# Kernel optimization log

Hardware: AMD Instinct MI355X
Metric: run time of the kernel (lower is better)

Reference implementation:

```python
import jax, jax.numpy as jnp
import numpy as np

B, T, E, H = 2, 2048, 4096, 32
D = E // H
NEG = -1e4  # additive causal mask value


def setup_inputs() -> dict:
    key = jax.random.key(0)
    ks = jax.random.split(key, 10)
    i8 = lambda k, shape: jax.random.randint(k, shape, -128, 128, dtype=jnp.int8)
    hidden_states = i8(ks[0], (B, T, E))
    W_q, b_q = i8(ks[1], (E, E)), i8(ks[2], (E,))
    W_k, b_k = i8(ks[3], (E, E)), i8(ks[4], (E,))
    W_v, b_v = i8(ks[5], (E, E)), i8(ks[6], (E,))
    W_o = i8(ks[7], (E, E))
    b_o = jax.random.normal(ks[8], (E,), jnp.float32)
    causal = jnp.where(jnp.tril(jnp.ones((T, T), bool)), 0.0, NEG).astype(jnp.float32)
    attention_mask = jnp.broadcast_to(causal[None, None], (B, 1, T, T))
    return {
        'hidden_states': hidden_states,
        'W_q': W_q, 'b_q': b_q, 'W_k': W_k, 'b_k': b_k,
        'W_v': W_v, 'b_v': b_v, 'W_o': W_o, 'b_o': b_o,
        'attention_mask': attention_mask,
        # dequant scales chosen so int8 outputs stay in range
        'a_q': jnp.float32(1e-4), 'a_k': jnp.float32(1e-4), 'a_v': jnp.float32(1e-4),
        'a_qk': jnp.float32(2e-5), 'a_pv': jnp.float32(1e-2), 'a_o': jnp.float32(1e-3),
    }


def _w8a8b8o8(x_i8, W_i8, b_i8, alpha):
    # int8 GEMM, int32 accumulate, fused scale+int8 bias, saturate to int8
    acc = jnp.einsum('bte,oe->bto', x_i8.astype(jnp.int32), W_i8.astype(jnp.int32))
    y = acc.astype(jnp.float32) * alpha + b_i8.astype(jnp.float32)
    return jnp.clip(jnp.round(y), -128, 127).astype(jnp.int8)


def _heads(x):  # [B,T,E] -> [B,H,T,D]
    return x.reshape(B, T, H, D).transpose(0, 2, 1, 3)


def reference(hidden_states, W_q, b_q, W_k, b_k, W_v, b_v, W_o, b_o,
              attention_mask, a_q, a_k, a_v, a_qk, a_pv, a_o):
    q = _heads(_w8a8b8o8(hidden_states, W_q, b_q, a_q))
    k = _heads(_w8a8b8o8(hidden_states, W_k, b_k, a_k))
    v = _heads(_w8a8b8o8(hidden_states, W_v, b_v, a_v))

    # BMM_S8T_S8N_F32T: fp32 logits = a_qk * int32(q @ k^T)
    logits = a_qk * jnp.einsum('bhtd,bhsd->bhts',
                               q.astype(jnp.int32), k.astype(jnp.int32)).astype(jnp.float32)
    logits = logits + attention_mask  # broadcast over heads
    probs = jax.nn.softmax(logits, axis=-1)
    p_i8 = jnp.round(probs * 127.0).astype(jnp.int8)  # attn_probs.mul_(127).round_()

    # BMM_S8T_S8N_S8T: int8 ctx = sat(round(a_pv * int32(p @ v)))
    ctx_acc = jnp.einsum('bhts,bhsd->bhtd',
                         p_i8.astype(jnp.int32), v.astype(jnp.int32)).astype(jnp.float32)
    ctx = jnp.clip(jnp.round(a_pv * ctx_acc), -128, 127).astype(jnp.int8)
    ctx = ctx.transpose(0, 2, 1, 3).reshape(B, T, E)

    # W8A8BFP32OFP32: fp32 out = a_o * int32(ctx @ W_o^T) + b_o
    out_acc = jnp.einsum('bte,oe->bto',
                         ctx.astype(jnp.int32), W_o.astype(jnp.int32)).astype(jnp.float32)
    return a_o * out_acc + b_o
```

## Files before the change

kernel.cpp:

```cpp
#include <hip/hip_runtime.h>

#define Bdim 2
#define Tdim 2048
#define Edim 4096
#define Hdim 32
#define Ddim 128
#define Mdim (Bdim*Tdim)
#define Kdim 4096

typedef int v4i __attribute__((ext_vector_type(4)));

__device__ __forceinline__ void glds16(const void* g, void* l) {
  __builtin_amdgcn_global_load_lds(
      (const __attribute__((address_space(1))) void*)g,
      (__attribute__((address_space(3))) void*)l, 16, 0, 0);
}

__global__ __launch_bounds__(256) void pack5_kernel(
    const int* __restrict__ s0, const int* __restrict__ s1, const int* __restrict__ s2,
    const int* __restrict__ s3, const int* __restrict__ s4,
    char* __restrict__ d0, char* __restrict__ d1, char* __restrict__ d2,
    char* __restrict__ d3, char* __restrict__ d4) {
  int which = blockIdx.y;
  const int* s = which == 0 ? s0 : which == 1 ? s1 : which == 2 ? s2 : which == 3 ? s3 : s4;
  char* d = which == 0 ? d0 : which == 1 ? d1 : which == 2 ? d2 : which == 3 ? d3 : d4;
  int i = blockIdx.x * 256 + threadIdx.x;
  int4 x = ((const int4*)s)[i];
  char4 y; y.x = (char)x.x; y.y = (char)x.y; y.z = (char)x.z; y.w = (char)x.w;
  ((char4*)d)[i] = y;
}

__global__ __launch_bounds__(256) void transpose_v(const char* __restrict__ V8,
                                                   char* __restrict__ Vt) {
  int bh = blockIdx.z, b = bh >> 5, h = bh & 31;
  int s0 = blockIdx.x * 64, d0 = blockIdx.y * 64;
  __shared__ __align__(16) char tl[64 * 80];
  int idx = threadIdx.x;
  {
    int row = idx >> 2, off = (idx & 3) * 16;
    v4i v = *(const v4i*)(V8 + (size_t)(b * Tdim + s0 + row) * Edim + h * Ddim + d0 + off);
    *(v4i*)(tl + row * 80 + off) = v;
  }
  __syncthreads();
  {
    int drow = idx >> 2, soff = (idx & 3) * 16;
    char out[16];
#pragma unroll
    for (int j = 0; j < 16; j++) out[j] = tl[(soff + j) * 80 + drow];
    *(v4i*)(Vt + ((size_t)bh * Ddim + d0 + drow) * Tdim + s0 + soff) = *(v4i*)out;
  }
}

template<int OUT_MODE>
__global__ __launch_bounds__(512, 2) void gemm_nt_i8(
    const char* __restrict__ A, const char* __restrict__ Bw,
    const int* __restrict__ bias_i, const float* __restrict__ bias_f,
    const float* __restrict__ alpha_p,
    char* __restrict__ out8, float* __restrict__ outf)
{
  const float alpha = alpha_p[0];
  asm volatile("s_waitcnt vmcnt(0)" ::: "memory");

  const int tid = threadIdx.x;
  const int wave = tid >> 6, lane = tid & 63;
  const int quad = lane >> 4, l16 = lane & 15;
  const int wr = wave >> 2, wc = wave & 3;

  const int wg = blockIdx.x;
  const int xcd = wg & 7, sl = wg >> 3;
  const int bm = (xcd >> 1) * 4 + (sl >> 3);
  const int bn = (xcd & 1) * 8 + (sl & 7);
  const int m0 = bm * 256, n0 = bn * 256;

  __shared__ __align__(16) char sm[3][2][16384];

  const char* asrc[2]; const char* bsrc[2]; int lo[2];
#pragma unroll
  for (int j = 0; j < 2; j++) {
    int cidx = j * 512 + tid;
    int row = cidx >> 2, q = cidx & 3;
    asrc[j] = A  + (size_t)(m0 + row) * Kdim + q * 16;
    bsrc[j] = Bw + (size_t)(n0 + row) * Kdim + q * 16;
    lo[j] = cidx * 16;
  }

  const int aoff = (wr * 128 + l16) * 64 + quad * 16;
  const int boff = (wc * 64  + l16) * 64 + quad * 16;

  v4i acc[8][4];
#pragma unroll
  for (int i = 0; i < 8; i++)
#pragma unroll
    for (int c = 0; c < 4; c++) acc[i][c] = (v4i){0, 0, 0, 0};

#pragma unroll
  for (int j = 0; j < 2; j++) glds16(asrc[j],      &sm[0][0][lo[j]]);
#pragma unroll
  for (int j = 0; j < 2; j++) glds16(bsrc[j],      &sm[0][1][lo[j]]);
#pragma unroll
  for (int j = 0; j < 2; j++) glds16(asrc[j] + 64, &sm[1][0][lo[j]]);
#pragma unroll
  for (int j = 0; j < 2; j++) glds16(bsrc[j] + 64, &sm[1][1][lo[j]]);

  int cur = 0, nxt = 2;
  for (int kt = 0; kt < 64; ++kt) {
    const char* As = &sm[cur][0][0];
    const char* Bs = &sm[cur][1][0];
    char* Ad = &sm[nxt][0][0];
    char* Bd = &sm[nxt][1][0];
    const int koff = (kt + 2) * 64;

    if (kt < 63) asm volatile("s_waitcnt vmcnt(4)" ::: "memory");
    else         asm volatile("s_waitcnt vmcnt(0)" ::: "memory");
    __builtin_amdgcn_s_barrier();
    __builtin_amdgcn_sched_barrier(0);

    v4i af[4], bf[4];
#pragma unroll
    for (int i = 0; i < 4; i++) af[i] = *(const v4i*)(As + aoff + i * 1024);
#pragma unroll
    for (int c = 0; c < 4; c++) bf[c] = *(const v4i*)(Bs + boff + c * 1024);
    if (kt < 62) {
      glds16(asrc[0] + koff, Ad + lo[0]);
      glds16(asrc[1] + koff, Ad + lo[1]);
    }
    __builtin_amdgcn_s_barrier();
    __builtin_amdgcn_s_setprio(1);
#pragma unroll
    for (int i = 0; i < 4; i++)
#pragma unroll
      for (int c = 0; c < 4; c++)
        acc[i][c] = __builtin_amdgcn_mfma_i32_16x16x64_i8(af[i], bf[c], acc[i][c], 0, 0, 0);
    __builtin_amdgcn_s_setprio(0);

#pragma unroll
    for (int i = 0; i < 4; i++) af[i] = *(const v4i*)(As + aoff + 4096 + i * 1024);
    if (kt < 62) {
      glds16(bsrc[0] + koff, Bd + lo[0]);
      glds16(bsrc[1] + koff, Bd + lo[1]);
    }
    __builtin_amdgcn_s_barrier();
    __builtin_amdgcn_s_setprio(1);
#pragma unroll
    for (int i = 0; i < 4; i++)
#pragma unroll
      for (int c = 0; c < 4; c++)
        acc[4 + i][c] = __builtin_amdgcn_mfma_i32_16x16x64_i8(af[i], bf[c], acc[4 + i][c], 0, 0, 0);
    __builtin_amdgcn_s_setprio(0);

    cur = cur == 2 ? 0 : cur + 1;
    nxt = nxt == 2 ? 0 : nxt + 1;
  }

#pragma unroll
  for (int mi = 0; mi < 8; mi++) {
#pragma unroll
    for (int c = 0; c < 4; c++) {
      int gcol = n0 + wc * 64 + c * 16 + l16;
#pragma unroll
      for (int r = 0; r < 4; r++) {
        int grow = m0 + wr * 128 + mi * 16 + quad * 4 + r;
        float y = (float)acc[mi][c][r] * alpha;
        if (OUT_MODE == 0) {
          y += (float)bias_i[gcol];
          int qv = (int)rintf(y);
          qv = qv < -128 ? -128 : (qv > 127 ? 127 : qv);
          out8[(size_t)grow * 4096 + gcol] = (char)qv;
        } else {
          outf[(size_t)grow * 4096 + gcol] = y + bias_f[gcol];
        }
      }
    }
  }
}

__global__ __launch_bounds__(256) void attn_kernel(
    const char* __restrict__ Q, const char* __restrict__ Kc, const char* __restrict__ Vt,
    const float* __restrict__ aqk_p, const float* __restrict__ apv_p,
    char* __restrict__ CTX)
{
  const int tid = threadIdx.x;
  const int wave = tid >> 6, lane = tid & 63;
  const int quad = lane >> 4, l16 = lane & 15;
  const int bh = blockIdx.y, b = bh >> 5, h = bh & 31;
  const int t0 = (gridDim.x - 1 - blockIdx.x) * 64;
  const int ntiles = (t0 >> 6) + 1;
  const float a_qk = aqk_p[0], a_pv = apv_p[0];

  __shared__ __align__(16) char qs[64 * 128];
  __shared__ __align__(16) char ks[64 * 128];
  __shared__ __align__(16) char vts[128 * 64];
  __shared__ __align__(16) char ps[4][16 * 80];

  const int t = t0 + 16 * wave + l16;
  const int h7 = l16 & 7;

#pragma unroll
  for (int j = 0; j < 2; j++) {
    int idx = tid + j * 256;
    int row = idx >> 3, ch = idx & 7;
    v4i v = *(const v4i*)(Q + (size_t)(b * Tdim + t0 + row) * Edim + h * Ddim + ch * 16);
    *(v4i*)(qs + row * 128 + ((ch ^ (row & 7)) * 16)) = v;
  }
  __syncthreads();
  v4i qB[2];
#pragma unroll
  for (int kk = 0; kk < 2; kk++)
    qB[kk] = *(const v4i*)(qs + (wave * 16 + l16) * 128 + (((4 * kk + quad) ^ h7) * 16));

  float m_run = -1e30f, l_run = 0.f;

  for (int it = 0; it < ntiles; ++it) {
    int s0 = it * 64;
    __syncthreads();
#pragma unroll
    for (int j = 0; j < 2; j++) {
      int idx = tid + j * 256;
      int row = idx >> 3, ch = idx & 7;
      v4i v = *(const v4i*)(Kc + (size_t)(b * Tdim + s0 + row) * Edim + h * Ddim + ch * 16);
      *(v4i*)(ks + row * 128 + ((ch ^ (row & 7)) * 16)) = v;
    }
    __syncthreads();

    float sv[4][4];
#pragma unroll
    for (int c = 0; c < 4; c++) {
      v4i acc = (v4i){0, 0, 0, 0};
#pragma unroll
      for (int kk = 0; kk < 2; kk++) {
        v4i aK = *(const v4i*)(ks + (16 * c + l16) * 128 + (((4 * kk + quad) ^ h7) * 16));
        acc = __builtin_amdgcn_mfma_i32_16x16x64_i8(aK, qB[kk], acc, 0, 0, 0);
      }
#pragma unroll
      for (int r = 0; r < 4; r++) {
        int s = s0 + 16 * c + 4 * quad + r;
        sv[c][r] = (s <= t) ? (float)acc[r] * a_qk : -1e30f;
      }
    }
    float mt = -1e30f;
#pragma unroll
    for (int c = 0; c < 4; c++)
#pragma unroll
      for (int r = 0; r < 4; r++) mt = fmaxf(mt, sv[c][r]);
    mt = fmaxf(mt, __shfl_xor(mt, 16));
    mt = fmaxf(mt, __shfl_xor(mt, 32));
    float mn = fmaxf(m_run, mt);
    float ss = 0.f;
#pragma unroll
    for (int c = 0; c < 4; c++)
#pragma unroll
      for (int r = 0; r < 4; r++) ss += __expf(sv[c][r] - mn);
    ss += __shfl_xor(ss, 16);
    ss += __shfl_xor(ss, 32);
    l_run = l_run * __expf(m_run - mn) + ss;
    m_run = mn;
  }

  const float rl = 127.0f / l_run;

  v4i accd[8];
#pragma unroll
  for (int dt = 0; dt < 8; dt++) accd[dt] = (v4i){0, 0, 0, 0};

  for (int it = 0; it < ntiles; ++it) {
    int s0 = it * 64;
    __syncthreads();
#pragma unroll
    for (int j = 0; j < 2; j++) {
      int idx = tid + j * 256;
      int row = idx >> 3, ch = idx & 7;
      v4i v = *(const v4i*)(Kc + (size_t)(b * Tdim + s0 + row) * Edim + h * Ddim + ch * 16);
      *(v4i*)(ks + row * 128 + ((ch ^ (row & 7)) * 16)) = v;
    }
#pragma unroll
    for (int j = 0; j < 2; j++) {
      int cidx = (wave * 2 + j) * 64 + lane;
      int row = cidx >> 2, off = (cidx & 3) * 16;
      glds16(Vt + ((size_t)bh * Ddim + row) * Tdim + s0 + off, vts + cidx * 16);
    }
    __syncthreads();

#pragma unroll
    for (int c = 0; c < 4; c++) {
      v4i acc = (v4i){0, 0, 0, 0};
#pragma unroll
      for (int kk = 0; kk < 2; kk++) {
        v4i aK = *(const v4i*)(ks + (16 * c + l16) * 128 + (((4 * kk + quad) ^ h7) * 16));
        acc = __builtin_amdgcn_mfma_i32_16x16x64_i8(aK, qB[kk], acc, 0, 0, 0);
      }
      char4 pc;
#pragma unroll
      for (int r = 0; r < 4; r++) {
        int s = s0 + 16 * c + 4 * quad + r;
        float p = 0.f;
        if (s <= t)
          p = rintf(__expf((float)acc[r] * a_qk - m_run) * rl);
        ((char*)&pc)[r] = (char)(int)p;
      }
      *(char4*)(ps[wave] + l16 * 80 + 16 * c + 4 * quad) = pc;
    }
    asm volatile("s_waitcnt lgkmcnt(0)" ::: "memory");
    v4i bP = *(const v4i*)(ps[wave] + l16 * 80 + quad * 16);
#pragma unroll
    for (int dt = 0; dt < 8; dt++) {
      v4i aV = *(const v4i*)(vts + (16 * dt + l16) * 64 + quad * 16);
      accd[dt] = __builtin_amdgcn_mfma_i32_16x16x64_i8(aV, bP, accd[dt], 0, 0, 0);
    }
  }

  size_t obase = (size_t)(b * Tdim + t) * Edim + h * Ddim;
#pragma unroll
  for (int dt = 0; dt < 8; dt++) {
    char4 oc;
#pragma unroll
    for (int r = 0; r < 4; r++) {
      int q = (int)rintf(a_pv * (float)accd[dt][r]);
      q = q < -128 ? -128 : (q > 127 ? 127 : q);
      ((char*)&oc)[r] = (char)q;
    }
    *(char4*)(CTX + obase + 16 * dt + 4 * quad) = oc;
  }
}

extern "C" void kernel_launch(void* const* d_in, const int* in_sizes, int n_in,
                              void* d_out, int out_size, void* d_ws, size_t ws_size,
                              hipStream_t stream) {
  const int*   hs  = (const int*)d_in[0];
  const int*   Wq  = (const int*)d_in[1];
  const int*   bq  = (const int*)d_in[2];
  const int*   Wk  = (const int*)d_in[3];
  const int*   bk  = (const int*)d_in[4];
  const int*   Wv  = (const int*)d_in[5];
  const int*   bv  = (const int*)d_in[6];
  const int*   Wo  = (const int*)d_in[7];
  const float* bo  = (const float*)d_in[8];
  const float* aq  = (const float*)d_in[10];
  const float* ak  = (const float*)d_in[11];
  const float* av  = (const float*)d_in[12];
  const float* aqk = (const float*)d_in[13];
  const float* apv = (const float*)d_in[14];
  const float* ao  = (const float*)d_in[15];

  char* ws = (char*)d_ws;
  const size_t SZ = (size_t)Mdim * Edim;
  char* h8   = ws + 0 * SZ;
  char* wq8  = ws + 1 * SZ;
  char* wk8  = ws + 2 * SZ;
  char* wv8  = ws + 3 * SZ;
  char* wo8  = ws + 4 * SZ;
  char* q8   = ws + 5 * SZ;
  char* k8   = ws + 6 * SZ;
  char* v8   = ws + 7 * SZ;
  char* vt8  = wq8;
  char* ctx8 = h8;

  pack5_kernel<<<dim3(16384, 5), 256, 0, stream>>>(hs, Wq, Wk, Wv, Wo,
                                                   h8, wq8, wk8, wv8, wo8);

  gemm_nt_i8<0><<<dim3(256), 512, 0, stream>>>(h8, wq8, bq, nullptr, aq, q8, nullptr);
  gemm_nt_i8<0><<<dim3(256), 512, 0, stream>>>(h8, wk8, bk, nullptr, ak, k8, nullptr);
  gemm_nt_i8<0><<<dim3(256), 512, 0, stream>>>(h8, wv8, bv, nullptr, av, v8, nullptr);

  transpose_v<<<dim3(32, 2, 64), 256, 0, stream>>>(v8, vt8);

  attn_kernel<<<dim3(32, 64), 256, 0, stream>>>(q8, k8, vt8, aqk, apv, ctx8);

  gemm_nt_i8<1><<<dim3(256), 512, 0, stream>>>(ctx8, wo8, nullptr, bo, ao, nullptr, (float*)d_out);
}
```

Baseline: 840.0 us.

## Merge GEMM k-loop MFMA phases and remap attention blocks across XCDs

```diff
diff --git a/kernel.cpp b/kernel.cpp
--- a/kernel.cpp
+++ b/kernel.cpp
@@ -115,37 +115,33 @@
     __builtin_amdgcn_s_barrier();
     __builtin_amdgcn_sched_barrier(0);
 
-    v4i af[4], bf[4];
-#pragma unroll
-    for (int i = 0; i < 4; i++) af[i] = *(const v4i*)(As + aoff + i * 1024);
-#pragma unroll
-    for (int c = 0; c < 4; c++) bf[c] = *(const v4i*)(Bs + boff + c * 1024);
+    v4i af0[4], af1[4], bf[4];
+#pragma unroll
+    for (int i = 0; i < 4; i++) af0[i] = *(const v4i*)(As + aoff + i * 1024);
+#pragma unroll
+    for (int c = 0; c < 4; c++) bf[c]  = *(const v4i*)(Bs + boff + c * 1024);
     if (kt < 62) {
       glds16(asrc[0] + koff, Ad + lo[0]);
       glds16(asrc[1] + koff, Ad + lo[1]);
     }
-    __builtin_amdgcn_s_barrier();
-    __builtin_amdgcn_s_setprio(1);
-#pragma unroll
-    for (int i = 0; i < 4; i++)
-#pragma unroll
-      for (int c = 0; c < 4; c++)
-        acc[i][c] = __builtin_amdgcn_mfma_i32_16x16x64_i8(af[i], bf[c], acc[i][c], 0, 0, 0);
-    __builtin_amdgcn_s_setprio(0);
-
-#pragma unroll
-    for (int i = 0; i < 4; i++) af[i] = *(const v4i*)(As + aoff + 4096 + i * 1024);
+#pragma unroll
+    for (int i = 0; i < 4; i++) af1[i] = *(const v4i*)(As + aoff + 4096 + i * 1024);
     if (kt < 62) {
       glds16(bsrc[0] + koff, Bd + lo[0]);
       glds16(bsrc[1] + koff, Bd + lo[1]);
     }
-    __builtin_amdgcn_s_barrier();
+
     __builtin_amdgcn_s_setprio(1);
 #pragma unroll
     for (int i = 0; i < 4; i++)
 #pragma unroll
       for (int c = 0; c < 4; c++)
-        acc[4 + i][c] = __builtin_amdgcn_mfma_i32_16x16x64_i8(af[i], bf[c], acc[4 + i][c], 0, 0, 0);
+        acc[i][c] = __builtin_amdgcn_mfma_i32_16x16x64_i8(af0[i], bf[c], acc[i][c], 0, 0, 0);
+#pragma unroll
+    for (int i = 0; i < 4; i++)
+#pragma unroll
+      for (int c = 0; c < 4; c++)
+        acc[4 + i][c] = __builtin_amdgcn_mfma_i32_16x16x64_i8(af1[i], bf[c], acc[4 + i][c], 0, 0, 0);
     __builtin_amdgcn_s_setprio(0);
 
     cur = cur == 2 ? 0 : cur + 1;
@@ -182,8 +178,12 @@
   const int tid = threadIdx.x;
   const int wave = tid >> 6, lane = tid & 63;
   const int quad = lane >> 4, l16 = lane & 15;
-  const int bh = blockIdx.y, b = bh >> 5, h = bh & 31;
-  const int t0 = (gridDim.x - 1 - blockIdx.x) * 64;
+
+  const int lin = blockIdx.y * 32 + blockIdx.x;
+  const int xcd = lin & 7, j = lin >> 3;
+  const int bh = xcd + 8 * (j >> 5);
+  const int b = bh >> 5, h = bh & 31;
+  const int t0 = (31 - (j & 31)) * 64;
   const int ntiles = (t0 >> 6) + 1;
   const float a_qk = aqk_p[0], a_pv = apv_p[0];
 
@@ -196,8 +196,8 @@
   const int h7 = l16 & 7;
 
 #pragma unroll
-  for (int j = 0; j < 2; j++) {
-    int idx = tid + j * 256;
+  for (int j2 = 0; j2 < 2; j2++) {
+    int idx = tid + j2 * 256;
     int row = idx >> 3, ch = idx & 7;
     v4i v = *(const v4i*)(Q + (size_t)(b * Tdim + t0 + row) * Edim + h * Ddim + ch * 16);
     *(v4i*)(qs + row * 128 + ((ch ^ (row & 7)) * 16)) = v;
@@ -214,8 +214,8 @@
     int s0 = it * 64;
     __syncthreads();
 #pragma unroll
-    for (int j = 0; j < 2; j++) {
-      int idx = tid + j * 256;
+    for (int j2 = 0; j2 < 2; j2++) {
+      int idx = tid + j2 * 256;
       int row = idx >> 3, ch = idx & 7;
       v4i v = *(const v4i*)(Kc + (size_t)(b * Tdim + s0 + row) * Edim + h * Ddim + ch * 16);
       *(v4i*)(ks + row * 128 + ((ch ^ (row & 7)) * 16)) = v;
@@ -266,15 +266,15 @@
     int s0 = it * 64;
     __syncthreads();
 #pragma unroll
-    for (int j = 0; j < 2; j++) {
-      int idx = tid + j * 256;
+    for (int j2 = 0; j2 < 2; j2++) {
+      int idx = tid + j2 * 256;
       int row = idx >> 3, ch = idx & 7;
       v4i v = *(const v4i*)(Kc + (size_t)(b * Tdim + s0 + row) * Edim + h * Ddim + ch * 16);
       *(v4i*)(ks + row * 128 + ((ch ^ (row & 7)) * 16)) = v;
     }
 #pragma unroll
-    for (int j = 0; j < 2; j++) {
-      int cidx = (wave * 2 + j) * 64 + lane;
+    for (int j2 = 0; j2 < 2; j2++) {
+      int cidx = (wave * 2 + j2) * 64 + lane;
       int row = cidx >> 2, off = (cidx & 3) * 16;
       glds16(Vt + ((size_t)bh * Ddim + row) * Tdim + s0 + off, vts + cidx * 16);
     }
```

New measurement: 759.6 us. 9.6% less time.
